# Optimization experiments

Hardware: AMD Instinct MI355X
Metric: run time of the kernel (lower is better)

## Reference

```python
import jax, jax.numpy as jnp
import numpy as np


def _conv2d(x, w, pad):
    return jax.lax.conv_general_dilated(
        x, w, (1, 1), [(pad, pad), (pad, pad)],
        dimension_numbers=('NCHW', 'OIHW', 'NCHW'))


def _affine_grid(theta, k):
    # torch F.affine_grid, align_corners=False; output size (k, k)
    base = ((2.0 * jnp.arange(k) + 1.0) / k - 1.0).astype(jnp.float32)
    pts = jnp.stack([
        jnp.broadcast_to(base[None, :], (k, k)),  # x varies along width
        jnp.broadcast_to(base[:, None], (k, k)),  # y varies along height
        jnp.ones((k, k), jnp.float32)], -1)        # [k,k,3]
    return jnp.einsum('ijc,nrc->nijr', pts, theta)  # [N,k,k,2] -> (x,y)


def _grid_sample(img, grid):
    # torch F.grid_sample: bilinear, zeros padding, align_corners=False
    # img [C,H,W], grid [k,k,2] with (x,y) in [-1,1]
    C, H, W = img.shape
    gx = (grid[..., 0] + 1.0) * W * 0.5 - 0.5
    gy = (grid[..., 1] + 1.0) * H * 0.5 - 0.5
    x0 = jnp.floor(gx); y0 = jnp.floor(gy)
    wx = gx - x0; wy = gy - y0
    x0i = x0.astype(jnp.int32); y0i = y0.astype(jnp.int32)

    def gath(yi, xi):
        valid = ((xi >= 0) & (xi < W) & (yi >= 0) & (yi < H)).astype(img.dtype)
        v = img[:, jnp.clip(yi, 0, H - 1), jnp.clip(xi, 0, W - 1)]  # [C,k,k]
        return v * valid[None]

    v00 = gath(y0i, x0i); v01 = gath(y0i, x0i + 1)
    v10 = gath(y0i + 1, x0i); v11 = gath(y0i + 1, x0i + 1)
    return (v00 * ((1 - wx) * (1 - wy))[None] + v01 * (wx * (1 - wy))[None]
            + v10 * ((1 - wx) * wy)[None] + v11 * (wx * wy)[None])


def reference(x, stn0_w, stn0_b, stn1_w, lin_w, lin_b, check):
    B, C, H, W = x.shape
    k = stn1_w.shape[-1]
    h = jax.nn.relu(_conv2d(x, stn0_w, k // 2) + stn0_b[None, :, None, None])
    ident6 = jnp.array([1., 0., 0., 0., 1., 0.], jnp.float32)
    out = _conv2d(h, stn1_w, 0) * (1.0 - check) + ident6[None, :, None, None]
    Ho, Wo = out.shape[2], out.shape[3]
    N = B * Ho * Wo
    # permute(0,3,2,1).view(N,2,3) as in torch
    theta = out.transpose(0, 3, 2, 1).reshape(N, 2, 3)
    grid = _affine_grid(theta, k)  # [N,k,k,2]
    xv = jnp.arange(k // 2, k // 2 + Ho, dtype=jnp.float32)[:, None]  # meshgrid 'ij'
    yv = jnp.arange(k // 2, k // 2 + Wo, dtype=jnp.float32)[None, :]
    half = float(k // 2)
    auxx = ((grid[..., 0] * half).reshape(B, Ho, Wo, k, k)
            + xv[None, :, :, None, None]).reshape(N, k, k) / (H - 1) * 2.0 - 1.0
    auxy = ((grid[..., 1] * half).reshape(B, Ho, Wo, k, k)
            + yv[None, :, :, None, None]).reshape(N, k, k) / (W - 1) * 2.0 - 1.0
    auxgrid = jnp.stack([auxx, auxy], -1).reshape(B, Ho * Wo, k, k, 2)
    # tile(x,0,Ho*Wo) duplicates x[b] for each of its Ho*Wo grids; gather directly
    xs = jax.vmap(lambda img, g: jax.vmap(lambda gg: _grid_sample(img, gg))(g))(x, auxgrid)  # [B,P,C,k,k]
    x_out = xs.reshape(N, -1) @ lin_w.T + lin_b  # [N,O]
    score = x_out.reshape(B, Ho, Wo, -1).transpose(0, 3, 2, 1)  # [B,O,Wo,Ho] as in torch
    ident23 = jnp.array([[1., 0., 0.], [0., 1., 0.]], jnp.float32)
    return score, ident23[None] - theta, out, auxx, auxy


def setup_inputs() -> dict:
    key = jax.random.key(0)
    ks = jax.random.split(key, 6)
    C, O, k = 128, 256, 3
    B, H, W = 8, 56, 56
    x = jax.random.normal(ks[0], (B, C, H, W), jnp.float32)
    stn0_w = jax.random.normal(ks[1], (C, C, k, k), jnp.float32) * (1.0 / np.sqrt(C * k * k))
    stn0_b = jax.random.normal(ks[2], (C,), jnp.float32) * 0.01
    # original zero-inits stn1; use small random so theta is non-trivial
    stn1_w = jax.random.normal(ks[3], (6, C, k, k), jnp.float32) * 0.01
    lin_w = jax.random.normal(ks[4], (O, C * k * k), jnp.float32) * (1.0 / np.sqrt(C * k * k))
    lin_b = jax.random.normal(ks[5], (O,), jnp.float32) * 0.01
    return {'x': x, 'stn0_w': stn0_w, 'stn0_b': stn0_b, 'stn1_w': stn1_w,
            'lin_w': lin_w, 'lin_b': lin_b, 'check': 0}
```

## Files before the change

### kernel.cpp

```cpp
#include <hip/hip_runtime.h>

typedef __attribute__((ext_vector_type(4))) float f32x4;
typedef __attribute__((ext_vector_type(8))) short bf16x8;

#define OPLANE 2916
#define NN 23328
#define KDIM 1152
#define PLANE 3136
#define LDP 72

__device__ __forceinline__ unsigned short f2bf(float f) {
    unsigned u = __builtin_bit_cast(unsigned, f);
    u += 0x7fffu + ((u >> 16) & 1u);
    return (unsigned short)(u >> 16);
}

__global__ __launch_bounds__(256) void k_pre(const float* __restrict__ x,
                                             const float* __restrict__ w0,
                                             const float* __restrict__ lw,
                                             unsigned short* __restrict__ xnh,
                                             unsigned short* __restrict__ b1t,
                                             unsigned short* __restrict__ b2t) {
    __shared__ unsigned short lds[56 * 132];
    if (blockIdx.x < 1728) {
        int idx = blockIdx.x * 256 + threadIdx.x;
        if (idx < 147456) {
            int r = idx / KDIM, k = idx - r * KDIM;
            int ij = k >> 7, ic = k & 127;
            b1t[idx] = f2bf(w0[r * KDIM + ic * 9 + ij]);
        } else {
            int j = idx - 147456;
            int r = j / KDIM, k = j - r * KDIM;
            int ij = k >> 7, ic = k & 127;
            b2t[j] = f2bf(lw[r * KDIM + ic * 9 + ij]);
        }
    } else {
        const int bid = blockIdx.x - 1728;
        const int y = bid % 56, b = bid / 56, tid = threadIdx.x;
        for (int i = tid; i < 7168; i += 256) {
            int ic = i / 56, xc = i - ic * 56;
            lds[xc * 132 + ic] = f2bf(x[(b * 128 + ic) * PLANE + y * 56 + xc]);
        }
        __syncthreads();
        for (int i = tid; i < 7168; i += 256) {
            int xc = i >> 7, ic = i & 127;
            xnh[(b * PLANE + y * 56 + xc) * 128 + ic] = lds[xc * 132 + ic];
        }
    }
}

__global__ __launch_bounds__(512) void k_gemm1(const unsigned short* __restrict__ xnh,
                                               const unsigned short* __restrict__ Bt,
                                               const float* __restrict__ bias,
                                               float* __restrict__ C) {
    __shared__ unsigned short As[64 * LDP];
    __shared__ unsigned short Bs[128 * LDP];
    const int tid = threadIdx.x;
    const int lane = tid & 63, wid = tid >> 6;
    const int wr = wid >> 2, wc = wid & 3;
    const int m0 = blockIdx.x * 64;

    f32x4 acc[2][2];
    #pragma unroll
    for (int mt = 0; mt < 2; mt++)
        #pragma unroll
        for (int nt = 0; nt < 2; nt++) { acc[mt][nt][0]=0.f; acc[mt][nt][1]=0.f; acc[mt][nt][2]=0.f; acc[mt][nt][3]=0.f; }

    const int row = tid >> 3, q = tid & 7;
    const int p = m0 + row;
    const int b = p / PLANE; int rem = p - b * PLANE;
    const int y = rem / 56; const int xc = rem - y * 56;
    unsigned short* asw = &As[row * LDP + q * 8];
    const int brow = tid >> 2, bq = tid & 3;
    const unsigned short* bg = Bt + brow * KDIM + bq * 16;
    unsigned short* bsw = &Bs[brow * LDP + bq * 16];
    const int lm = lane & 15, lq = lane >> 4;

    uint4 a0, bv0, bv1;
    auto issue = [&](int it) {
        const int ij = it >> 1;
        const int di = ij / 3, dj = ij - di * 3;
        const int icb = (it & 1) << 6;
        a0 = make_uint4(0u,0u,0u,0u);
        bool valid = (y + di >= 1) && (y + di <= 56) && (xc + dj >= 1) && (xc + dj <= 56);
        if (valid) {
            const unsigned short* ap = xnh + (p + (di - 1) * 56 + (dj - 1)) * 128 + icb + q * 8;
            a0 = *(const uint4*)ap;
        }
        bv0 = *(const uint4*)(bg + it * 64);
        bv1 = *(const uint4*)(bg + it * 64 + 8);
    };
    issue(0);

    #pragma unroll
    for (int it = 0; it < 18; it++) {
        __syncthreads();
        *(uint4*)asw = a0;
        *(uint4*)(bsw + 0) = bv0; *(uint4*)(bsw + 8) = bv1;
        __syncthreads();
        if (it < 17) issue(it + 1);
        #pragma unroll
        for (int kk = 0; kk < 64; kk += 32) {
            bf16x8 af[2], bf[2];
            #pragma unroll
            for (int mt = 0; mt < 2; mt++)
                af[mt] = *(const bf16x8*)&As[(wr * 32 + mt * 16 + lm) * LDP + kk + lq * 8];
            #pragma unroll
            for (int nt = 0; nt < 2; nt++)
                bf[nt] = *(const bf16x8*)&Bs[(wc * 32 + nt * 16 + lm) * LDP + kk + lq * 8];
            #pragma unroll
            for (int mt = 0; mt < 2; mt++)
                #pragma unroll
                for (int nt = 0; nt < 2; nt++)
                    acc[mt][nt] = __builtin_amdgcn_mfma_f32_16x16x32_bf16(af[mt], bf[nt], acc[mt][nt], 0, 0, 0);
        }
    }
    #pragma unroll
    for (int mt = 0; mt < 2; mt++) {
        int m = m0 + wr * 32 + mt * 16 + lq * 4;
        #pragma unroll
        for (int nt = 0; nt < 2; nt++) {
            int n = wc * 32 + nt * 16 + lm;
            float bb = bias[n];
            #pragma unroll
            for (int r = 0; r < 4; r++)
                C[(m + r) * 128 + n] = fmaxf(acc[mt][nt][r] + bb, 0.f);
        }
    }
}

__global__ __launch_bounds__(256) void k_conv2f(const float* __restrict__ h,
                                                const float* __restrict__ w1,
                                                const int* __restrict__ check,
                                                float* __restrict__ o_out,
                                                float* __restrict__ o_th,
                                                float* __restrict__ o_ax,
                                                float* __restrict__ o_ay,
                                                float* __restrict__ sxy) {
    __shared__ float wlds[6912];
    __shared__ float red[16 * 6 * 17];
    __shared__ float vals[96];
    const int tid = threadIdx.x;
    for (int idx = tid; idx < 6912; idx += 256) {
        int r = idx / KDIM, k = idx - r * KDIM;
        int ij = k >> 7, ic = k & 127;
        wlds[idx] = w1[r * KDIM + ic * 9 + ij];
    }
    __syncthreads();
    const int pt = tid >> 4, c = tid & 15;
    const int p = blockIdx.x * 16 + pt;
    int b = p / OPLANE; int rem = p - b * OPLANE; int oh = rem / 54; int ow = rem - oh * 54;
    const float4* h4 = (const float4*)h;
    const float4* w4 = (const float4*)wlds;
    float acc[6] = {0.f, 0.f, 0.f, 0.f, 0.f, 0.f};
    const int base_sp = b * PLANE + oh * 56 + ow;
    #pragma unroll
    for (int i = 0; i < 3; i++) {
        #pragma unroll
        for (int j = 0; j < 3; j++) {
            int sp = base_sp + i * 56 + j;
            float4 h0 = h4[sp * 32 + c * 2];
            float4 h1 = h4[sp * 32 + c * 2 + 1];
            int ij = i * 3 + j;
            #pragma unroll
            for (int r = 0; r < 6; r++) {
                float4 wa = w4[r * 288 + ij * 32 + c * 2];
                float4 wb = w4[r * 288 + ij * 32 + c * 2 + 1];
                acc[r] += h0.x * wa.x + h0.y * wa.y + h0.z * wa.z + h0.w * wa.w
                        + h1.x * wb.x + h1.y * wb.y + h1.z * wb.z + h1.w * wb.w;
            }
        }
    }
    #pragma unroll
    for (int r = 0; r < 6; r++) red[(pt * 6 + r) * 17 + c] = acc[r];
    __syncthreads();
    if (tid < 96) {
        const float* rp = &red[tid * 17];
        float s = 0.f;
        #pragma unroll
        for (int e = 0; e < 16; e++) s += rp[e];
        vals[tid] = s;
    }
    __syncthreads();
    if (tid < 16) {
        int p2 = blockIdx.x * 16 + tid;
        int b2 = p2 / OPLANE; int r2 = p2 - b2 * OPLANE; int oh2 = r2 / 54; int ow2 = r2 - oh2 * 54;
        float val[6];
        float s = 1.0f - (float)check[0];
        const float id6[6] = {1.f, 0.f, 0.f, 0.f, 1.f, 0.f};
        #pragma unroll
        for (int r = 0; r < 6; r++) val[r] = vals[tid * 6 + r] * s + id6[r];
        int n = (b2 * 54 + ow2) * 54 + oh2;
        #pragma unroll
        for (int r = 0; r < 6; r++) {
            o_out[((b2 * 6 + r) * 54 + oh2) * 54 + ow2] = val[r];
            o_th[n * 6 + r] = id6[r] - val[r];
        }
        const float bse[3] = {-2.f / 3.f, 0.f, 2.f / 3.f};
        #pragma unroll
        for (int i = 0; i < 3; i++)
            #pragma unroll
            for (int j = 0; j < 3; j++) {
                float gx = bse[j] * val[0] + bse[i] * val[1] + val[2];
                float gy = bse[j] * val[3] + bse[i] * val[4] + val[5];
                float ax = (gx + 1.f + (float)ow2) * (2.f / 55.f) - 1.f;
                float ay = (gy + 1.f + (float)oh2) * (2.f / 55.f) - 1.f;
                int ij = i * 3 + j;
                o_ax[n * 9 + ij] = ax;
                o_ay[n * 9 + ij] = ay;
                sxy[(n * 9 + ij) * 2 + 0] = (ax + 1.f) * 28.f - 0.5f;
                sxy[(n * 9 + ij) * 2 + 1] = (ay + 1.f) * 28.f - 0.5f;
            }
    }
}

__global__ __launch_bounds__(256) void k_sgemm(const unsigned short* __restrict__ xnh,
                                               const unsigned short* __restrict__ Wt,
                                               const float* __restrict__ bias,
                                               const float* __restrict__ sxy,
                                               float* __restrict__ score) {
    __shared__ unsigned short Ss[64 * LDP];
    __shared__ unsigned short Ws[128 * LDP];
    const int tid = threadIdx.x;
    const int lane = tid & 63, wid = tid >> 6;
    const int wr = wid >> 1, wc = wid & 1;
    const int o0 = blockIdx.x * 128;
    const int s0 = blockIdx.y * 64;

    f32x4 acc[4][2];
    #pragma unroll
    for (int mt = 0; mt < 4; mt++)
        #pragma unroll
        for (int nt = 0; nt < 2; nt++) { acc[mt][nt][0]=0.f; acc[mt][nt][1]=0.f; acc[mt][nt][2]=0.f; acc[mt][nt][3]=0.f; }

    const int row = tid >> 2, q = tid & 3;
    const int mp = min(s0 + row, NN - 1);
    const int b = mp / OPLANE; const int rr = mp - b * OPLANE;
    const int ho = rr / 54, wo = rr - (rr / 54) * 54;
    const int n = (b * 54 + wo) * 54 + ho;
    const int xbase = b * PLANE;
    unsigned short* ssw = &Ss[row * LDP + q * 16];
    const int wrow = tid >> 1, wq = tid & 1;
    const unsigned short* wg = Wt + (o0 + wrow) * KDIM + wq * 32;
    unsigned short* wsw = &Ws[wrow * LDP + wq * 32];
    const int lm = lane & 15, lq = lane >> 4;

    float2 sc[9];
    {
        const float* spp = sxy + n * 18;
        #pragma unroll
        for (int ij = 0; ij < 9; ij++) sc[ij] = *(const float2*)(spp + ij * 2);
    }

    int off0 = 0, off1 = 0, off2 = 0, off3 = 0;
    float wt0 = 0.f, wt1 = 0.f, wt2 = 0.f, wt3 = 0.f;
    auto mkoff = [&](int ij) {
        float sx = sc[ij].x, sy = sc[ij].y;
        float x0f = floorf(sx), y0f = floorf(sy);
        float wx = sx - x0f, wy = sy - y0f;
        int x0 = (int)x0f, y0 = (int)y0f;
        int x1 = x0 + 1, y1 = y0 + 1;
        float vx0 = (x0 >= 0 && x0 < 56) ? 1.f : 0.f;
        float vx1 = (x1 >= 0 && x1 < 56) ? 1.f : 0.f;
        float vy0 = (y0 >= 0 && y0 < 56) ? 1.f : 0.f;
        float vy1 = (y1 >= 0 && y1 < 56) ? 1.f : 0.f;
        int xc0 = min(max(x0, 0), 55), xc1 = min(max(x1, 0), 55);
        int yc0 = min(max(y0, 0), 55), yc1 = min(max(y1, 0), 55);
        off0 = (xbase + yc0 * 56 + xc0) << 7;
        off1 = (xbase + yc0 * 56 + xc1) << 7;
        off2 = (xbase + yc1 * 56 + xc0) << 7;
        off3 = (xbase + yc1 * 56 + xc1) << 7;
        wt0 = vy0 * vx0 * (1.f - wx) * (1.f - wy);
        wt1 = vy0 * vx1 * wx * (1.f - wy);
        wt2 = vy1 * vx0 * (1.f - wx) * wy;
        wt3 = vy1 * vx1 * wx * wy;
    };

    uint4 p0a, p0b, p1a, p1b, p2a, p2b, p3a, p3b;
    uint4 w0v, w1v, w2v, w3v;
    auto issue = [&](int it) {
        const int co = ((it & 1) << 6) + q * 16;
        p0a = *(const uint4*)(xnh + off0 + co);
        p0b = *(const uint4*)(xnh + off0 + co + 8);
        p1a = *(const uint4*)(xnh + off1 + co);
        p1b = *(const uint4*)(xnh + off1 + co + 8);
        p2a = *(const uint4*)(xnh + off2 + co);
        p2b = *(const uint4*)(xnh + off2 + co + 8);
        p3a = *(const uint4*)(xnh + off3 + co);
        p3b = *(const uint4*)(xnh + off3 + co + 8);
        w0v = *(const uint4*)(wg + it * 64);
        w1v = *(const uint4*)(wg + it * 64 + 8);
        w2v = *(const uint4*)(wg + it * 64 + 16);
        w3v = *(const uint4*)(wg + it * 64 + 24);
    };

    mkoff(0);
    issue(0);

    #pragma unroll
    for (int it = 0; it < 18; it++) {
        unsigned dw[8];
        const unsigned* d0 = (const unsigned*)&p0a;
        const unsigned* d1 = (const unsigned*)&p1a;
        const unsigned* d2 = (const unsigned*)&p2a;
        const unsigned* d3 = (const unsigned*)&p3a;
        const unsigned* e0 = (const unsigned*)&p0b;
        const unsigned* e1 = (const unsigned*)&p1b;
        const unsigned* e2 = (const unsigned*)&p2b;
        const unsigned* e3 = (const unsigned*)&p3b;
        #pragma unroll
        for (int d = 0; d < 8; d++) {
            unsigned u0 = (d < 4) ? d0[d] : e0[d - 4];
            unsigned u1 = (d < 4) ? d1[d] : e1[d - 4];
            unsigned u2 = (d < 4) ? d2[d] : e2[d - 4];
            unsigned u3 = (d < 4) ? d3[d] : e3[d - 4];
            float lo = wt0 * __builtin_bit_cast(float, u0 << 16)
                     + wt1 * __builtin_bit_cast(float, u1 << 16)
                     + wt2 * __builtin_bit_cast(float, u2 << 16)
                     + wt3 * __builtin_bit_cast(float, u3 << 16);
            float hi = wt0 * __builtin_bit_cast(float, u0 & 0xffff0000u)
                     + wt1 * __builtin_bit_cast(float, u1 & 0xffff0000u)
                     + wt2 * __builtin_bit_cast(float, u2 & 0xffff0000u)
                     + wt3 * __builtin_bit_cast(float, u3 & 0xffff0000u);
            dw[d] = (unsigned)f2bf(lo) | ((unsigned)f2bf(hi) << 16);
        }
        __syncthreads();
        *(uint4*)(ssw + 0) = *(uint4*)&dw[0];
        *(uint4*)(ssw + 8) = *(uint4*)&dw[4];
        *(uint4*)(wsw + 0)  = w0v;
        *(uint4*)(wsw + 8)  = w1v;
        *(uint4*)(wsw + 16) = w2v;
        *(uint4*)(wsw + 24) = w3v;
        __syncthreads();
        if (it < 17) {
            if (((it + 1) & 1) == 0) mkoff((it + 1) >> 1);
            issue(it + 1);
        }
        #pragma unroll
        for (int kk = 0; kk < 64; kk += 32) {
            bf16x8 wf[4], sf[2];
            #pragma unroll
            for (int mt = 0; mt < 4; mt++)
                wf[mt] = *(const bf16x8*)&Ws[(wr * 64 + mt * 16 + lm) * LDP + kk + lq * 8];
            #pragma unroll
            for (int nt = 0; nt < 2; nt++)
                sf[nt] = *(const bf16x8*)&Ss[(wc * 32 + nt * 16 + lm) * LDP + kk + lq * 8];
            #pragma unroll
            for (int mt = 0; mt < 4; mt++)
                #pragma unroll
                for (int nt = 0; nt < 2; nt++)
                    acc[mt][nt] = __builtin_amdgcn_mfma_f32_16x16x32_bf16(wf[mt], sf[nt], acc[mt][nt], 0, 0, 0);
        }
    }
    #pragma unroll
    for (int mt = 0; mt < 4; mt++) {
        #pragma unroll
        for (int r = 0; r < 4; r++) {
            int o = o0 + wr * 64 + mt * 16 + lq * 4 + r;
            float bb = bias[o];
            #pragma unroll
            for (int nt = 0; nt < 2; nt++) {
                int s = s0 + wc * 32 + nt * 16 + lm;
                if (s < NN) {
                    int sb = s / OPLANE;
                    int soff = s - sb * OPLANE;
                    score[(sb * 256 + o) * OPLANE + soff] = acc[mt][nt][r] + bb;
                }
            }
        }
    }
}

extern "C" void kernel_launch(void* const* d_in, const int* in_sizes, int n_in,
                              void* d_out, int out_size, void* d_ws, size_t ws_size,
                              hipStream_t stream) {
    const float* x  = (const float*)d_in[0];
    const float* w0 = (const float*)d_in[1];
    const float* b0 = (const float*)d_in[2];
    const float* w1 = (const float*)d_in[3];
    const float* lw = (const float*)d_in[4];
    const float* lb = (const float*)d_in[5];
    const int* check = (const int*)d_in[6];

    float* out   = (float*)d_out;
    float* score = out;
    float* o_th  = out + 5971968;
    float* o_out = out + 6111936;
    float* o_ax  = out + 6251904;
    float* o_ay  = out + 6461856;

    char* wsb = (char*)d_ws;
    float* h   = (float*)wsb;
    unsigned short* xnh = (unsigned short*)(wsb + 12845056);
    unsigned short* b1t = (unsigned short*)(wsb + 19267584);
    unsigned short* b2t = (unsigned short*)(wsb + 19562496);
    float* sxy = (float*)(wsb + 20152320);

    k_pre<<<2176, 256, 0, stream>>>(x, w0, lw, xnh, b1t, b2t);
    k_gemm1<<<392, 512, 0, stream>>>(xnh, b1t, b0, h);
    k_conv2f<<<1458, 256, 0, stream>>>(h, w1, check, o_out, o_th, o_ax, o_ay, sxy);
    k_sgemm<<<dim3(2, 365), 256, 0, stream>>>(xnh, b2t, lb, sxy, score);
}
```

Before: 167.0 us.

## Store conv1 activations as bf16 and swizzle sampled-GEMM block order

The first conv GEMM now writes its ReLU output h as bf16 instead of fp32, and the second conv reads one 16-byte vector per position and unpacks it to floats. This halves the traffic for writing and reading h (about 12.8MB in fp32). The sampled GEMM launch is flattened to a 1D grid remapped in groups so both output-column tiles of a spatial tile run close together, which should improve L2 reuse of the gathered input. The cost is extra rounding in the theta-producing conv, which can shift the sampling coordinates.

After: 161.7 us. 3.2% less time.

```diff
diff --git a/kernel.cpp b/kernel.cpp
--- a/kernel.cpp
+++ b/kernel.cpp
@@ -13,6 +13,12 @@
     unsigned u = __builtin_bit_cast(unsigned, f);
     u += 0x7fffu + ((u >> 16) & 1u);
     return (unsigned short)(u >> 16);
+}
+__device__ __forceinline__ float bflo(unsigned u) {
+    return __builtin_bit_cast(float, u << 16);
+}
+__device__ __forceinline__ float bfhi(unsigned u) {
+    return __builtin_bit_cast(float, u & 0xffff0000u);
 }
 
 __global__ __launch_bounds__(256) void k_pre(const float* __restrict__ x,
@@ -52,7 +58,7 @@
 __global__ __launch_bounds__(512) void k_gemm1(const unsigned short* __restrict__ xnh,
                                                const unsigned short* __restrict__ Bt,
                                                const float* __restrict__ bias,
-                                               float* __restrict__ C) {
+                                               unsigned short* __restrict__ h) {
     __shared__ unsigned short As[64 * LDP];
     __shared__ unsigned short Bs[128 * LDP];
     const int tid = threadIdx.x;
@@ -124,12 +130,12 @@
             float bb = bias[n];
             #pragma unroll
             for (int r = 0; r < 4; r++)
-                C[(m + r) * 128 + n] = fmaxf(acc[mt][nt][r] + bb, 0.f);
-        }
-    }
-}
-
-__global__ __launch_bounds__(256) void k_conv2f(const float* __restrict__ h,
+                h[(m + r) * 128 + n] = f2bf(fmaxf(acc[mt][nt][r] + bb, 0.f));
+        }
+    }
+}
+
+__global__ __launch_bounds__(256) void k_conv2f(const unsigned short* __restrict__ h,
                                                 const float* __restrict__ w1,
                                                 const int* __restrict__ check,
                                                 float* __restrict__ o_out,
@@ -150,7 +156,7 @@
     const int pt = tid >> 4, c = tid & 15;
     const int p = blockIdx.x * 16 + pt;
     int b = p / OPLANE; int rem = p - b * OPLANE; int oh = rem / 54; int ow = rem - oh * 54;
-    const float4* h4 = (const float4*)h;
+    const uint4* h4 = (const uint4*)h;
     const float4* w4 = (const float4*)wlds;
     float acc[6] = {0.f, 0.f, 0.f, 0.f, 0.f, 0.f};
     const int base_sp = b * PLANE + oh * 56 + ow;
@@ -159,15 +165,18 @@
         #pragma unroll
         for (int j = 0; j < 3; j++) {
             int sp = base_sp + i * 56 + j;
-            float4 h0 = h4[sp * 32 + c * 2];
-            float4 h1 = h4[sp * 32 + c * 2 + 1];
+            uint4 hu = h4[sp * 16 + c];
+            float f0 = bflo(hu.x), f1 = bfhi(hu.x);
+            float f2 = bflo(hu.y), f3 = bfhi(hu.y);
+            float f4 = bflo(hu.z), f5 = bfhi(hu.z);
+            float f6 = bflo(hu.w), f7 = bfhi(hu.w);
             int ij = i * 3 + j;
             #pragma unroll
             for (int r = 0; r < 6; r++) {
                 float4 wa = w4[r * 288 + ij * 32 + c * 2];
                 float4 wb = w4[r * 288 + ij * 32 + c * 2 + 1];
-                acc[r] += h0.x * wa.x + h0.y * wa.y + h0.z * wa.z + h0.w * wa.w
-                        + h1.x * wb.x + h1.y * wb.y + h1.z * wb.z + h1.w * wb.w;
+                acc[r] += f0 * wa.x + f1 * wa.y + f2 * wa.z + f3 * wa.w
+                        + f4 * wb.x + f5 * wb.y + f6 * wb.z + f7 * wb.w;
             }
         }
     }
@@ -221,11 +230,16 @@
                                                float* __restrict__ score) {
     __shared__ unsigned short Ss[64 * LDP];
     __shared__ unsigned short Ws[128 * LDP];
+    const int i = blockIdx.x;
+    const int g = i >> 4, r16 = i & 15;
+    const int m8 = r16 >> 3;
+    const int pp = g * 8 + (r16 & 7);
+    if (pp >= 365) return;
+    const int o0 = m8 * 128;
+    const int s0 = pp * 64;
     const int tid = threadIdx.x;
     const int lane = tid & 63, wid = tid >> 6;
     const int wr = wid >> 1, wc = wid & 1;
-    const int o0 = blockIdx.x * 128;
-    const int s0 = blockIdx.y * 64;
 
     f32x4 acc[4][2];
     #pragma unroll
@@ -314,14 +328,8 @@
             unsigned u1 = (d < 4) ? d1[d] : e1[d - 4];
             unsigned u2 = (d < 4) ? d2[d] : e2[d - 4];
             unsigned u3 = (d < 4) ? d3[d] : e3[d - 4];
-            float lo = wt0 * __builtin_bit_cast(float, u0 << 16)
-                     + wt1 * __builtin_bit_cast(float, u1 << 16)
-                     + wt2 * __builtin_bit_cast(float, u2 << 16)
-                     + wt3 * __builtin_bit_cast(float, u3 << 16);
-            float hi = wt0 * __builtin_bit_cast(float, u0 & 0xffff0000u)
-                     + wt1 * __builtin_bit_cast(float, u1 & 0xffff0000u)
-                     + wt2 * __builtin_bit_cast(float, u2 & 0xffff0000u)
-                     + wt3 * __builtin_bit_cast(float, u3 & 0xffff0000u);
+            float lo = wt0 * bflo(u0) + wt1 * bflo(u1) + wt2 * bflo(u2) + wt3 * bflo(u3);
+            float hi = wt0 * bfhi(u0) + wt1 * bfhi(u1) + wt2 * bfhi(u2) + wt3 * bfhi(u3);
             dw[d] = (unsigned)f2bf(lo) | ((unsigned)f2bf(hi) << 16);
         }
         __syncthreads();
@@ -390,7 +398,7 @@
     float* o_ay  = out + 6461856;
 
     char* wsb = (char*)d_ws;
-    float* h   = (float*)wsb;
+    unsigned short* h   = (unsigned short*)wsb;
     unsigned short* xnh = (unsigned short*)(wsb + 12845056);
     unsigned short* b1t = (unsigned short*)(wsb + 19267584);
     unsigned short* b2t = (unsigned short*)(wsb + 19562496);
@@ -399,5 +407,5 @@
     k_pre<<<2176, 256, 0, stream>>>(x, w0, lw, xnh, b1t, b2t);
     k_gemm1<<<392, 512, 0, stream>>>(xnh, b1t, b0, h);
     k_conv2f<<<1458, 256, 0, stream>>>(h, w1, check, o_out, o_th, o_ax, o_ay, sxy);
-    k_sgemm<<<dim3(2, 365), 256, 0, stream>>>(xnh, b2t, lb, sxy, score);
-}
+    k_sgemm<<<736, 256, 0, stream>>>(xnh, b2t, lb, sxy, score);
+}
```
